# Optimization experiments

Measured on AMD Instinct MI355X. Metric: run time of the kernel, lower is better.

Reference implementation:

```python
import jax, jax.numpy as jnp
import numpy as np

B = 64        # graphs per batch
N_PER = 1024  # nodes per graph (equal-size graphs -> to_dense_batch mask is all-true)
C = 128       # in_channels
K = 64        # pooled clusters (k)
DEG = 32      # average degree
N = B * N_PER
E = N * DEG


def setup_inputs() -> dict:
    key = jax.random.key(0)
    k1, k2, k3, k4, k5 = jax.random.split(key, 5)
    x = jax.random.normal(k1, (N, C), dtype=jnp.float32)
    # edges constrained to stay within each graph (PyG batched-graph invariant)
    src_l = jax.random.randint(k2, (B, N_PER * DEG), 0, N_PER)
    dst_l = jax.random.randint(k3, (B, N_PER * DEG), 0, N_PER)
    off = (jnp.arange(B) * N_PER)[:, None]
    edge_index = jnp.stack([(src_l + off).reshape(-1), (dst_l + off).reshape(-1)], axis=0)
    batch = jnp.repeat(jnp.arange(B), N_PER)
    W_msg = jax.random.normal(k4, (C, K), dtype=jnp.float32) / np.float32(np.sqrt(C))
    W_root = jax.random.normal(k5, (C, K), dtype=jnp.float32) / np.float32(np.sqrt(C))
    b = jnp.zeros((K,), dtype=jnp.float32)
    return {"x": x, "edge_index": edge_index, "batch": batch,
            "W_msg": W_msg, "W_root": W_root, "b": b}


def reference(x, edge_index, batch, W_msg, W_root, b):
    src, dst = edge_index[0], edge_index[1]
    # ---- LSSMP: learned-score message passing -> cluster scores s [N, K] ----
    m = jax.nn.elu(x @ W_msg)                                  # per-node messages [N, K]
    agg = jax.ops.segment_sum(m[src], dst, num_segments=N)     # scatter-add over edges
    s = jnp.tanh(agg + x @ W_root + b)                         # act = tanh
    # ---- to_dense_batch (equal-size graphs: pure reshape, mask all-true) ----
    xd = x.reshape(B, N_PER, C)
    sd = s.reshape(B, N_PER, K)
    # ---- to_dense_adj ----
    g = src // N_PER
    adj = jnp.zeros((B, N_PER, N_PER), jnp.float32).at[g, src % N_PER, dst % N_PER].add(1.0)
    # ---- dense_connect: S = softmax(s); out = S^T X ; out_adj = S^T A S ----
    S = jax.nn.softmax(sd, axis=-1)                            # [B, N_PER, K]
    out = jnp.einsum('bnk,bnc->bkc', S, xd)                    # [B, K, C]
    out_adj = jnp.einsum('bkn,bnm,bml->bkl',
                         S.transpose(0, 2, 1), adj, S)         # [B, K, K]
    # ---- to_sparse_batch: pooled adjacency is dense -> all-pairs edges ----
    x_out = out.reshape(B * K, C)
    grid = jnp.stack(jnp.meshgrid(jnp.arange(K), jnp.arange(K), indexing='ij'), 0).reshape(2, -1)
    offs = (jnp.arange(B) * K)[None, :, None]
    edge_index_out = (grid[:, None, :] + offs).reshape(2, -1)  # [2, B*K*K]
    batch_out = jnp.repeat(jnp.arange(B), K)
    # original returns (x, edge_index, None, batch, None, None); adj values are dropped
    del out_adj
    return x_out, edge_index_out, batch_out
```

## Files before the change

kernel.cpp:

```cpp
#include <hip/hip_runtime.h>
#include <hip/hip_bf16.h>

typedef __hip_bfloat16 bf16;

#define NPER 1024
#define CC   128
#define KK   64
#define NTOT 65536
#define ETOT 2097152
#define EPG  32768
#define ESL  8192

#define M_OFF    0
#define R_OFF    8388608
#define SORT_OFF 16777216
#define RP_OFF   20971520
#define FLAG_OFF 21233664
#define ZB_OFF   21233728
#define WS_NEED  21233984ULL
#define WF_OFF   21233984
#define WS_NEED2 21266752ULL
#define GH_OFF   M_OFF
#define GC_OFF   (M_OFF + 2097152)

typedef short bf16x8 __attribute__((ext_vector_type(8)));
typedef _Float16 half8 __attribute__((ext_vector_type(8)));
typedef float f32x4 __attribute__((ext_vector_type(4)));

__device__ __forceinline__ float t15_rb(float v) {
    return __bfloat162float(__float2bfloat16(v));
}
__device__ __forceinline__ float t15_bf(unsigned short h) {
    unsigned int w = ((unsigned int)h) << 16;
    float f;
    __builtin_memcpy(&f, &w, 4);
    return f;
}
__device__ __forceinline__ unsigned short t15_f2b(float f) {
    bf16 h = __float2bfloat16(f);
    unsigned short u;
    __builtin_memcpy(&u, &h, 2);
    return u;
}

__device__ __forceinline__ int t15_src(const int* ei, int e, int mode) {
    return (mode == 2 ? ei[2 * e] : ei[e]) & 65535;
}
__device__ __forceinline__ int t15_dst(const int* ei, int e, int mode) {
    return (mode == 2 ? ei[2 * ETOT + 2 * e] : ei[ETOT + e]) & 65535;
}

__global__ __launch_bounds__(1024) void t15_hist(const int* __restrict__ ei,
                                                 int* __restrict__ ghist,
                                                 const float* __restrict__ Wm,
                                                 const float* __restrict__ Wr,
                                                 unsigned short* __restrict__ wf) {
    int t = threadIdx.x;
    int blk = blockIdx.x;
    if (blk == 256) {
        if (!wf) return;
        for (int idx = t; idx < 16384; idx += 1024) {
            int w = idx >> 13;
            int r = idx & 8191;
            int fr = r >> 3;
            int j = r & 7;
            int lane = fr & 63;
            int sc = fr >> 6;
            int step = sc >> 2, ct = sc & 3;
            int c = step * 32 + 8 * (lane >> 4) + j;
            int kk = ct * 16 + (lane & 15);
            const float* W = w ? Wr : Wm;
            wf[idx] = t15_f2b(W[c * 64 + kk]);
        }
        return;
    }
    __shared__ int hist[2048];
    __shared__ int sdet[1024];
    __shared__ int smode;
    int ebase = blk * ESL;
    sdet[t] = ei[2 * (ebase + t) + 1];
    __syncthreads();
    for (int off = 512; off; off >>= 1) {
        if (t < off) sdet[t] |= sdet[t + off];
        __syncthreads();
    }
    if (t == 0) smode = (sdet[0] != 0) ? 1 : 2;
    hist[t] = 0;
    hist[t + 1024] = 0;
    __syncthreads();
    int mode = smode;
    for (int i = t; i < ESL; i += 1024) {
        int e = ebase + i;
        int s = t15_src(ei, e, mode) & (NPER - 1);
        int d = t15_dst(ei, e, mode) & (NPER - 1);
        atomicAdd(&hist[(d << 1) | ((s >> 9) & 1)], 1);
    }
    __syncthreads();
    ghist[blk * 2048 + t] = hist[t];
    ghist[blk * 2048 + 1024 + t] = hist[t + 1024];
}

__global__ __launch_bounds__(1024) void t15_scan(const int* __restrict__ ghist,
                                                 int* __restrict__ gcur,
                                                 unsigned short* __restrict__ rowptr,
                                                 float* __restrict__ zbias) {
    __shared__ int sh[8192];
    __shared__ int sscan[1024];
    int t = threadIdx.x, g = blockIdx.x;
    if (g == 0 && t < 64) zbias[t] = 0.f;
    for (int i = t; i < 8192; i += 1024) sh[i] = ghist[g * 8192 + i];
    __syncthreads();
    int b0 = 2 * t, b1 = 2 * t + 1;
    int h0[4], h1[4];
    int c0 = 0, c1 = 0;
#pragma unroll
    for (int q = 0; q < 4; ++q) {
        h0[q] = sh[q * 2048 + b0]; c0 += h0[q];
        h1[q] = sh[q * 2048 + b1]; c1 += h1[q];
    }
    int ts = c0 + c1;
    sscan[t] = ts;
    __syncthreads();
    for (int off = 1; off < 1024; off <<= 1) {
        int v = sscan[t];
        int a = (t >= off) ? sscan[t - off] : 0;
        __syncthreads();
        sscan[t] = v + a;
        __syncthreads();
    }
    int incl = sscan[t], excl = incl - ts;
    rowptr[g * 2048 + b0] = (unsigned short)(excl + c0);
    rowptr[g * 2048 + b1] = (unsigned short)incl;
    int r0 = excl, r1 = excl + c0;
#pragma unroll
    for (int q = 0; q < 4; ++q) {
        gcur[(g * 4 + q) * 2048 + b0] = r0; r0 += h0[q];
        gcur[(g * 4 + q) * 2048 + b1] = r1; r1 += h1[q];
    }
}

__global__ __launch_bounds__(1024) void t15_scat(const int* __restrict__ ei,
                                                 const int* __restrict__ gcur,
                                                 unsigned short* __restrict__ sorted) {
    __shared__ int cur[2048];
    __shared__ int sdet[1024];
    __shared__ int smode;
    int t = threadIdx.x, blk = blockIdx.x;
    int ebase = blk * ESL;
    int g = blk >> 2;
    sdet[t] = ei[2 * (ebase + t) + 1];
    __syncthreads();
    for (int off = 512; off; off >>= 1) {
        if (t < off) sdet[t] |= sdet[t + off];
        __syncthreads();
    }
    if (t == 0) smode = (sdet[0] != 0) ? 1 : 2;
    cur[t] = gcur[blk * 2048 + t];
    cur[t + 1024] = gcur[blk * 2048 + 1024 + t];
    __syncthreads();
    int mode = smode;
    unsigned short* sg = sorted + g * EPG;
    for (int i = t; i < ESL; i += 1024) {
        int e = ebase + i;
        int s = t15_src(ei, e, mode) & (NPER - 1);
        int d = t15_dst(ei, e, mode) & (NPER - 1);
        int pos = atomicAdd(&cur[(d << 1) | ((s >> 9) & 1)], 1);
        if ((unsigned)pos < (unsigned)EPG) sg[pos] = (unsigned short)s;
    }
}

__global__ __launch_bounds__(256) void t15_mroot_mfma(
        const float* __restrict__ x, const unsigned short* __restrict__ wf,
        const float* __restrict__ bias,
        bf16* __restrict__ m_out, bf16* __restrict__ root_out) {
    __shared__ unsigned short sX[64 * CC];
    int t = threadIdx.x;
    int lane = t & 63;
    int wv = t >> 6;
    int ww = wv & 1;
    int ct0 = (wv >> 1) * 2;
    int rl = lane & 15, g2 = lane >> 4;

    bf16x8 bq[4][2];
    const uint4* wfq = (const uint4*)wf;
#pragma unroll
    for (int step = 0; step < 4; ++step)
#pragma unroll
        for (int cti = 0; cti < 2; ++cti) {
            uint4 u = wfq[(size_t)(((ww * 4 + step) * 4) + ct0 + cti) * 64 + lane];
            bq[step][cti] = __builtin_bit_cast(bf16x8, u);
        }
    float bv0 = bias[ct0 * 16 + rl];
    float bv1 = bias[ct0 * 16 + 16 + rl];
    bf16* dst = ww ? root_out : m_out;

    for (int ti = 0; ti < 2; ++ti) {
        int tile = blockIdx.x * 2 + ti;
        size_t rowbase = (size_t)tile * 64;
        if (ti) __syncthreads();
        const float4* xg = (const float4*)(x + rowbase * CC);
        for (int i = t; i < 2048; i += 256) {
            float4 v = xg[i];
            int row = i >> 5;
            int cb = (i & 31) * 8;
            int addr = row * 256 + (cb ^ ((row & 7) << 4));
            ushort4 h;
            h.x = t15_f2b(v.x); h.y = t15_f2b(v.y);
            h.z = t15_f2b(v.z); h.w = t15_f2b(v.w);
            *(ushort4*)((char*)sX + addr) = h;
        }
        __syncthreads();

        for (int rt = 0; rt < 4; ++rt) {
            int row = rt * 16 + rl;
            bf16x8 af[4];
#pragma unroll
            for (int step = 0; step < 4; ++step) {
                int addr = row * 256 + ((g2 * 16 + step * 64) ^ ((row & 7) << 4));
                uint4 u = *(const uint4*)((const char*)sX + addr);
                af[step] = __builtin_bit_cast(bf16x8, u);
            }
            f32x4 acc0 = {0.f, 0.f, 0.f, 0.f};
            f32x4 acc1 = {0.f, 0.f, 0.f, 0.f};
#pragma unroll
            for (int step = 0; step < 4; ++step) {
                acc0 = __builtin_amdgcn_mfma_f32_16x16x32_bf16(af[step], bq[step][0], acc0, 0, 0, 0);
                acc1 = __builtin_amdgcn_mfma_f32_16x16x32_bf16(af[step], bq[step][1], acc1, 0, 0, 0);
            }
            int n0 = (int)rowbase + rt * 16 + g2 * 4;
#pragma unroll
            for (int cti = 0; cti < 2; ++cti) {
                f32x4 a = cti ? acc1 : acc0;
                float bv = cti ? bv1 : bv0;
                int kk = (ct0 + cti) * 16 + rl;
#pragma unroll
                for (int r = 0; r < 4; ++r) {
                    float v = a[r];
                    if (ww) v += bv;
                    else    v = v > 0.f ? v : expm1f(v);
                    dst[(size_t)(n0 + r) * KK + kk] = __float2bfloat16(v);
                }
            }
        }
    }
}

__global__ void t15_mroot(const float* __restrict__ x, const float* __restrict__ Wm,
                          const float* __restrict__ Wr, const float* __restrict__ bias,
                          bf16* __restrict__ m_out, bf16* __restrict__ root_out) {
    __shared__ bf16 sWm[CC * KK];
    __shared__ bf16 sWr[CC * KK];
    __shared__ bf16 sX[64 * CC];
    int t = threadIdx.x;
    int nb = blockIdx.x * 64;
    for (int i = t; i < CC * KK; i += 256) {
        sWm[i] = __float2bfloat16(Wm[i]);
        sWr[i] = __float2bfloat16(Wr[i]);
    }
    const float4* xg = (const float4*)(x + (size_t)nb * CC);
    for (int i = t; i < (64 * CC) / 4; i += 256) {
        float4 v = xg[i];
        sX[i * 4 + 0] = __float2bfloat16(v.x);
        sX[i * 4 + 1] = __float2bfloat16(v.y);
        sX[i * 4 + 2] = __float2bfloat16(v.z);
        sX[i * 4 + 3] = __float2bfloat16(v.w);
    }
    int k = t & 63, rg = t >> 6;
    float bv = bias[k];
    __syncthreads();
    float accm[16], accr[16];
#pragma unroll
    for (int r = 0; r < 16; ++r) { accm[r] = 0.f; accr[r] = 0.f; }
    for (int c = 0; c < CC; ++c) {
        float wm = __bfloat162float(sWm[c * KK + k]);
        float wr = __bfloat162float(sWr[c * KK + k]);
#pragma unroll
        for (int r = 0; r < 16; ++r) {
            float xv = __bfloat162float(sX[(rg + 4 * r) * CC + c]);
            accm[r] += xv * wm;
            accr[r] += xv * wr;
        }
    }
#pragma unroll
    for (int r = 0; r < 16; ++r) {
        int n = nb + rg + 4 * r;
        float mv = accm[r];
        mv = mv > 0.f ? mv : expm1f(mv);
        m_out[(size_t)n * KK + k] = __float2bfloat16(mv);
        root_out[(size_t)n * KK + k] = __float2bfloat16(accr[r] + bv);
    }
}

__global__ __launch_bounds__(512, 4) void t15_gatherlds(
        const unsigned short* __restrict__ rowptr,
        const unsigned short* __restrict__ sorted_src,
        const unsigned short* __restrict__ m_in,
        bf16* __restrict__ rootS) {
    __shared__ unsigned short sM[512 * KK];
    int lane = threadIdx.x & 63;
    int wv = threadIdx.x >> 6;
    int g = blockIdx.x >> 3;
    int nl0 = (blockIdx.x & 7) * 128 + wv * 16;
    int nbase = g * NPER + nl0;
    const unsigned short* rp = rowptr + g * 2048;
    const unsigned short* idx = sorted_src + g * EPG;
    int b0 = 2 * nl0;

    unsigned rpv = 0;
    if (lane <= 32 && (b0 + lane) > 0) rpv = (unsigned)rp[b0 + lane - 1];

    float acc[16];
#pragma unroll
    for (int nn = 0; nn < 16; ++nn)
        acc[nn] = t15_bf(((const unsigned short*)rootS)[(size_t)(nbase + nn) * KK + lane]);

#pragma unroll
    for (int h = 0; h < 2; ++h) {
        unsigned vi[16];
#pragma unroll
        for (int nn = 0; nn < 16; ++nn) {
            int bb = 2 * nn + h;
            int s = (int)__builtin_amdgcn_readlane(rpv, bb);
            int e = (int)__builtin_amdgcn_readlane(rpv, bb + 1);
            if (s > EPG) s = EPG;
            if (e < s) e = s;
            if (e > EPG) e = EPG;
            int w0 = s >> 1;
            int wc = ((e + 1) >> 1) - w0;
            if (wc > 64) wc = 64;
            unsigned v = 0;
            if (lane < wc) v = *(const unsigned*)(idx + 2 * (w0 + lane));
            vi[nn] = v;
        }
        if (h) __syncthreads();
        const uint4* mg = (const uint4*)(m_in + ((size_t)g * NPER + h * 512) * KK);
        uint4* ml = (uint4*)sM;
        for (int i = threadIdx.x; i < (512 * KK) / 8; i += 512) ml[i] = mg[i];
        __syncthreads();

#pragma unroll
        for (int nn = 0; nn < 16; ++nn) {
            int bb = 2 * nn + h;
            int s = (int)__builtin_amdgcn_readlane(rpv, bb);
            int e = (int)__builtin_amdgcn_readlane(rpv, bb + 1);
            if (s > EPG) s = EPG;
            if (e < s) e = s;
            if (e > EPG) e = EPG;
            int w0 = s >> 1;
            int wc = ((e + 1) >> 1) - w0;
            if (wc > 64) wc = 64;
            float a0 = acc[nn], a1 = 0.f;
            int i = s;
            if (i < e && (i & 1)) {
                unsigned w = __builtin_amdgcn_readlane(vi[nn], 0);
                a0 += t15_bf(sM[((w >> 16) & 511u) * KK + lane]);
                ++i;
            }
            int elim = 2 * (w0 + wc);
            if (elim > e) elim = e;
            for (; i + 2 <= elim; i += 2) {
                unsigned w = __builtin_amdgcn_readlane(vi[nn], (i >> 1) - w0);
                a0 += t15_bf(sM[(w & 511u) * KK + lane]);
                a1 += t15_bf(sM[((w >> 16) & 511u) * KK + lane]);
            }
            if (i < elim) {
                unsigned w = __builtin_amdgcn_readlane(vi[nn], (i >> 1) - w0);
                a0 += t15_bf(sM[(w & 511u) * KK + lane]);
                ++i;
            }
            for (; i < e; ++i) {
                unsigned sv = __builtin_amdgcn_readfirstlane((unsigned)idx[i]);
                a0 += t15_bf(sM[(sv & 511u) * KK + lane]);
            }
            acc[nn] = a0 + a1;
        }
    }

#pragma unroll
    for (int nn = 0; nn < 16; ++nn) {
        float sv = tanhf(acc[nn]);
        float mx = sv;
        for (int o = 32; o; o >>= 1) mx = fmaxf(mx, __shfl_xor(mx, o, 64));
        float ev = expf(sv - mx);
        float sm = ev;
        for (int o = 32; o; o >>= 1) sm += __shfl_xor(sm, o, 64);
        rootS[(size_t)(nbase + nn) * KK + lane] = __float2bfloat16(ev / sm);
    }
}

__global__ __launch_bounds__(512) void t15_pool_mfma(
        const float* __restrict__ x, const bf16* __restrict__ S_in,
        float* __restrict__ outp) {
    __shared__ char sP[24576];
    int tt = threadIdx.x;
    int lane = tt & 63;
    int wv = tt >> 6;
    int mt = wv & 3;
    int nt = wv >> 2;
    int rl = lane & 15, g2 = lane >> 4;
    int g = blockIdx.x >> 2;
    int cq = (blockIdx.x & 3) * 32;

    f32x4 acc = {0.f, 0.f, 0.f, 0.f};

    for (int tile = 0; tile < 8; ++tile) {
        size_t nbase = (size_t)g * NPER + tile * 128;
        if (tile) __syncthreads();
        const uint2* sg = (const uint2*)(S_in + nbase * KK);
        for (int i = 0; i < 4; ++i) {
            int idx = tt + 512 * i;
            int r = idx >> 4;
            int q = idx & 15;
            uint2 u = sg[idx];
            unsigned short b[4] = {(unsigned short)(u.x & 0xffff),
                                   (unsigned short)(u.x >> 16),
                                   (unsigned short)(u.y & 0xffff),
                                   (unsigned short)(u.y >> 16)};
#pragma unroll
            for (int j = 0; j < 4; ++j) {
                int k = 4 * q + j;
                _Float16 h = (_Float16)t15_bf(b[j]);
                *(_Float16*)(sP + k * 256 + ((2 * r) ^ ((k & 7) << 4))) = h;
            }
        }
        const float* xb = x + nbase * CC + cq;
        for (int i = 0; i < 2; ++i) {
            int idx = tt + 512 * i;
            int r = idx >> 3;
            int q = idx & 7;
            float4 v = *(const float4*)(xb + (size_t)r * CC + 4 * q);
#pragma unroll
            for (int j = 0; j < 4; ++j) {
                int c = 4 * q + j;
                float fv = (j == 0) ? v.x : (j == 1) ? v.y : (j == 2) ? v.z : v.w;
                _Float16 h = (_Float16)fv;
                *(_Float16*)(sP + 16384 + c * 256 + ((2 * r) ^ ((c & 7) << 4))) = h;
            }
        }
        __syncthreads();
#pragma unroll
        for (int ks = 0; ks < 4; ++ks) {
            int nb2 = 2 * (32 * ks + 8 * g2);
            int arow = 16 * mt + rl;
            uint4 ua = *(const uint4*)(sP + arow * 256 + (nb2 ^ ((arow & 7) << 4)));
            int brow = 16 * nt + rl;
            uint4 ub = *(const uint4*)(sP + 16384 + brow * 256 + (nb2 ^ ((brow & 7) << 4)));
            half8 A = __builtin_bit_cast(half8, ua);
            half8 B = __builtin_bit_cast(half8, ub);
            acc = __builtin_amdgcn_mfma_f32_16x16x32_f16(A, B, acc, 0, 0, 0);
        }
    }

#pragma unroll
    for (int r = 0; r < 4; ++r) {
        int krow = 16 * mt + 4 * g2 + r;
        outp[(size_t)(g * KK + krow) * CC + cq + 16 * nt + rl] = t15_rb(acc[r]);
    }
}

__global__ void t15_edgefill(float* __restrict__ outp) {
    int gid = blockIdx.x * 256 + threadIdx.x;
    if (gid >= 528384) return;
    float val;
    if (gid < 524288) {
        int r = gid >> 18;
        int rem = gid & 262143;
        int b = rem >> 12;
        int p = rem & 4095;
        int v = (r == 0) ? (p >> 6) : (p & 63);
        val = (float)(v + b * 64);
    } else {
        val = (float)((gid - 524288) >> 6);
    }
    outp[524288 + gid] = t15_rb(val);
}

extern "C" void kernel_launch(void* const* d_in, const int* in_sizes, int n_in,
                              void* d_out, int out_size, void* d_ws, size_t ws_size,
                              hipStream_t stream) {
    const float* x = nullptr; const int* ei = nullptr;
    const float* Wm = nullptr; const float* Wr = nullptr; const float* bias = nullptr;
    for (int i = 0; i < n_in; ++i) {
        int s = in_sizes[i];
        if (s == 8388608 && !x)       x  = (const float*)d_in[i];
        else if (s == 4194304 && !ei) ei = (const int*)d_in[i];
        else if (s == 8192) { if (!Wm) Wm = (const float*)d_in[i]; else if (!Wr) Wr = (const float*)d_in[i]; }
        else if (s == 64 && !bias)    bias = (const float*)d_in[i];
    }
    if (!x)  x  = (const float*)d_in[0];
    if (!ei) ei = (const int*)d_in[1];
    if (!Wm && n_in > 3) Wm = (const float*)d_in[3];
    if (!Wr && n_in > 4) Wr = (const float*)d_in[4];

    float* outp = (float*)d_out;
    bool out_ok = (out_size >= 1052672);
    bool ws_ok  = (ws_size >= WS_NEED) && x && ei && Wm && Wr;
    bool wf_ok  = (ws_size >= WS_NEED2);

    if (out_ok) {
        t15_edgefill<<<2064, 256, 0, stream>>>(outp);
    }
    if (out_ok && ws_ok) {
        char* ws = (char*)d_ws;
        bf16*           m_buf  = (bf16*)(ws + M_OFF);
        bf16*           rootS  = (bf16*)(ws + R_OFF);
        unsigned short* sorted = (unsigned short*)(ws + SORT_OFF);
        unsigned short* rowptr = (unsigned short*)(ws + RP_OFF);
        float*          zbias  = (float*)(ws + ZB_OFF);
        unsigned short* wf     = wf_ok ? (unsigned short*)(ws + WF_OFF) : nullptr;
        int*            ghist  = (int*)(ws + GH_OFF);
        int*            gcur   = (int*)(ws + GC_OFF);
        const float* bz = bias ? bias : zbias;

        t15_hist<<<257, 1024, 0, stream>>>(ei, ghist, Wm, Wr, wf);
        t15_scan<<<64, 1024, 0, stream>>>(ghist, gcur, rowptr, zbias);
        t15_scat<<<256, 1024, 0, stream>>>(ei, gcur, sorted);
        if (wf_ok)
            t15_mroot_mfma<<<512, 256, 0, stream>>>(x, wf, bz, m_buf, rootS);
        else
            t15_mroot<<<NTOT / 64, 256, 0, stream>>>(x, Wm, Wr, bz, m_buf, rootS);
        t15_gatherlds<<<512, 512, 0, stream>>>(rowptr, sorted,
                                               (const unsigned short*)m_buf, rootS);
        t15_pool_mfma<<<256, 512, 0, stream>>>(x, rootS, outp);
    }
}
```

Before: 202.2 us.

## Split gather edges across half-waves with packed bf16 loads; fuse edge fill into pool

The gather kernel now has each 32-lane half of a wavefront read one packed pair of bf16 channels per LDS load. The two halves take alternate source nodes of each edge pair and are combined with a cross-half shuffle before the tanh/softmax, which halves per-edge LDS reads and softmax shuffle steps. The separate edge-index fill kernel is folded into extra blocks of the pooling kernel, saving one launch. Added costs are more register pressure from two accumulator arrays and some masking overhead on the odd-edge paths.

```diff
diff --git a/kernel.cpp b/kernel.cpp
--- a/kernel.cpp
+++ b/kernel.cpp
@@ -297,6 +297,7 @@
         const unsigned short* __restrict__ m_in,
         bf16* __restrict__ rootS) {
     __shared__ unsigned short sM[512 * KK];
+    const unsigned* sM32 = (const unsigned*)sM;
     int lane = threadIdx.x & 63;
     int wv = threadIdx.x >> 6;
     int g = blockIdx.x >> 3;
@@ -305,14 +306,21 @@
     const unsigned short* rp = rowptr + g * 2048;
     const unsigned short* idx = sorted_src + g * EPG;
     int b0 = 2 * nl0;
+    int l31 = lane & 31;
+    bool hi = lane >= 32;
 
     unsigned rpv = 0;
     if (lane <= 32 && (b0 + lane) > 0) rpv = (unsigned)rp[b0 + lane - 1];
 
-    float acc[16];
-#pragma unroll
-    for (int nn = 0; nn < 16; ++nn)
-        acc[nn] = t15_bf(((const unsigned short*)rootS)[(size_t)(nbase + nn) * KK + lane]);
+    float accL[16], accH[16];
+    const unsigned* rS32 = (const unsigned*)rootS;
+#pragma unroll
+    for (int nn = 0; nn < 16; ++nn) {
+        unsigned pr = rS32[(size_t)(nbase + nn) * 32 + l31];
+        if (hi) pr = 0;
+        accL[nn] = t15_bf((unsigned short)(pr & 0xffffu));
+        accH[nn] = t15_bf((unsigned short)(pr >> 16));
+    }
 
 #pragma unroll
     for (int h = 0; h < 2; ++h) {
@@ -349,42 +357,59 @@
             int w0 = s >> 1;
             int wc = ((e + 1) >> 1) - w0;
             if (wc > 64) wc = 64;
-            float a0 = acc[nn], a1 = 0.f;
-            int i = s;
-            if (i < e && (i & 1)) {
-                unsigned w = __builtin_amdgcn_readlane(vi[nn], 0);
-                a0 += t15_bf(sM[((w >> 16) & 511u) * KK + lane]);
-                ++i;
-            }
             int elim = 2 * (w0 + wc);
             if (elim > e) elim = e;
-            for (; i + 2 <= elim; i += 2) {
-                unsigned w = __builtin_amdgcn_readlane(vi[nn], (i >> 1) - w0);
-                a0 += t15_bf(sM[(w & 511u) * KK + lane]);
-                a1 += t15_bf(sM[((w >> 16) & 511u) * KK + lane]);
-            }
-            if (i < elim) {
-                unsigned w = __builtin_amdgcn_readlane(vi[nn], (i >> 1) - w0);
-                a0 += t15_bf(sM[(w & 511u) * KK + lane]);
-                ++i;
-            }
-            for (; i < e; ++i) {
+            float aL = accL[nn], aH = accH[nn];
+            int j = 0;
+            if ((s & 1) && s < elim) {
+                unsigned w = __builtin_amdgcn_readlane(vi[nn], 0);
+                unsigned v = sM32[((w >> 16) & 511u) * 32 + l31];
+                if (hi) v = 0;
+                aL += t15_bf((unsigned short)(v & 0xffffu));
+                aH += t15_bf((unsigned short)(v >> 16));
+                j = 1;
+            }
+            int jfull = (elim >> 1) - w0;
+            for (; j < jfull; ++j) {
+                unsigned w = __builtin_amdgcn_readlane(vi[nn], j);
+                unsigned s0 = w & 511u;
+                unsigned s1 = (w >> 16) & 511u;
+                unsigned sel = hi ? s1 : s0;
+                unsigned v = sM32[sel * 32 + l31];
+                aL += t15_bf((unsigned short)(v & 0xffffu));
+                aH += t15_bf((unsigned short)(v >> 16));
+            }
+            if ((elim & 1) && elim > s) {
+                unsigned w = __builtin_amdgcn_readlane(vi[nn], jfull);
+                unsigned v = sM32[(w & 511u) * 32 + l31];
+                if (hi) v = 0;
+                aL += t15_bf((unsigned short)(v & 0xffffu));
+                aH += t15_bf((unsigned short)(v >> 16));
+            }
+            for (int i = elim; i < e; ++i) {
                 unsigned sv = __builtin_amdgcn_readfirstlane((unsigned)idx[i]);
-                a0 += t15_bf(sM[(sv & 511u) * KK + lane]);
-            }
-            acc[nn] = a0 + a1;
+                unsigned v = sM32[(sv & 511u) * 32 + l31];
+                if (hi) v = 0;
+                aL += t15_bf((unsigned short)(v & 0xffffu));
+                aH += t15_bf((unsigned short)(v >> 16));
+            }
+            accL[nn] = aL; accH[nn] = aH;
         }
     }
 
 #pragma unroll
     for (int nn = 0; nn < 16; ++nn) {
-        float sv = tanhf(acc[nn]);
-        float mx = sv;
-        for (int o = 32; o; o >>= 1) mx = fmaxf(mx, __shfl_xor(mx, o, 64));
-        float ev = expf(sv - mx);
-        float sm = ev;
-        for (int o = 32; o; o >>= 1) sm += __shfl_xor(sm, o, 64);
-        rootS[(size_t)(nbase + nn) * KK + lane] = __float2bfloat16(ev / sm);
+        float aL = accL[nn] + __shfl_xor(accL[nn], 32, 64);
+        float aH = accH[nn] + __shfl_xor(accH[nn], 32, 64);
+        float svL = tanhf(aL), svH = tanhf(aH);
+        float mx = fmaxf(svL, svH);
+        for (int o = 16; o; o >>= 1) mx = fmaxf(mx, __shfl_xor(mx, o, 64));
+        float eL = expf(svL - mx), eH = expf(svH - mx);
+        float sm = eL + eH;
+        for (int o = 16; o; o >>= 1) sm += __shfl_xor(sm, o, 64);
+        unsigned outw = (unsigned)t15_f2b(eL / sm) | ((unsigned)t15_f2b(eH / sm) << 16);
+        if (lane < 32)
+            ((unsigned*)rootS)[(size_t)(nbase + nn) * 32 + l31] = outw;
     }
 }
 
@@ -393,6 +418,23 @@
         float* __restrict__ outp) {
     __shared__ char sP[24576];
     int tt = threadIdx.x;
+    if (blockIdx.x >= 256) {
+        int gid = (blockIdx.x - 256) * 512 + tt;
+        if (gid >= 528384) return;
+        float val;
+        if (gid < 524288) {
+            int r = gid >> 18;
+            int rem = gid & 262143;
+            int b = rem >> 12;
+            int p = rem & 4095;
+            int v = (r == 0) ? (p >> 6) : (p & 63);
+            val = (float)(v + b * 64);
+        } else {
+            val = (float)((gid - 524288) >> 6);
+        }
+        outp[524288 + gid] = t15_rb(val);
+        return;
+    }
     int lane = tt & 63;
     int wv = tt >> 6;
     int mt = wv & 3;
@@ -497,7 +539,7 @@
     bool ws_ok  = (ws_size >= WS_NEED) && x && ei && Wm && Wr;
     bool wf_ok  = (ws_size >= WS_NEED2);
 
-    if (out_ok) {
+    if (out_ok && !ws_ok) {
         t15_edgefill<<<2064, 256, 0, stream>>>(outp);
     }
     if (out_ok && ws_ok) {
@@ -521,6 +563,6 @@
             t15_mroot<<<NTOT / 64, 256, 0, stream>>>(x, Wm, Wr, bz, m_buf, rootS);
         t15_gatherlds<<<512, 512, 0, stream>>>(rowptr, sorted,
                                                (const unsigned short*)m_buf, rootS);
-        t15_pool_mfma<<<256, 512, 0, stream>>>(x, rootS, outp);
-    }
-}
+        t15_pool_mfma<<<1288, 512, 0, stream>>>(x, rootS, outp);
+    }
+}
```

Measured after the change: 202.6 us. About the same (+0.2%).
